# Kernel optimization log

Measured on AMD Instinct MI355X. Metric: run time of the kernel, lower is better.

The kernel has to match this reference:

```python
import jax, jax.numpy as jnp
import numpy as np

N_NODES = 50000
N_EDGES = 800000
D = 64
LN_EPS = 1e-5


def setup_inputs() -> dict:
    key = jax.random.key(0)
    k1, k2, k3 = jax.random.split(key, 3)
    x = jax.random.normal(k1, (N_NODES, D), dtype=jnp.float32)
    edge_index = jax.random.randint(k2, (2, N_EDGES), 0, N_NODES, dtype=jnp.int64)
    # GCNConv linear weight (no bias in lin; conv bias separate), kaiming-ish scale
    W = jax.random.normal(k3, (D, D), dtype=jnp.float32) / np.sqrt(D)
    b = jnp.zeros((D,), dtype=jnp.float32)
    # LayerNorm affine params
    gamma = jnp.ones((D,), dtype=jnp.float32)
    beta = jnp.zeros((D,), dtype=jnp.float32)
    return {"x": x, "edge_index": edge_index, "W": W, "b": b, "gamma": gamma, "beta": beta}


def reference(x, edge_index, W, b, gamma, beta):
    n = x.shape[0]
    # --- GCNConv (normalize=True, improved=False, add_self_loops=True) ---
    loops = jnp.arange(n, dtype=edge_index.dtype)
    src = jnp.concatenate([edge_index[0], loops])  # message sources j
    dst = jnp.concatenate([edge_index[1], loops])  # message targets i
    ew = jnp.ones(src.shape[0], dtype=x.dtype)
    deg = jax.ops.segment_sum(ew, dst, num_segments=n)          # in-degree incl. self-loop
    dinv = jnp.where(deg > 0, jax.lax.rsqrt(jnp.where(deg > 0, deg, 1.0)), 0.0)
    norm = dinv[src] * dinv[dst]                                 # [E+N]
    xw = x @ W                                                   # [N, D]
    z = jax.ops.segment_sum(norm[:, None] * xw[src], dst, num_segments=n) + b
    # --- identity skip connection ---
    h = x + z
    # --- norm_act_drop: LayerNorm + ReLU (dropout_prob=0) ---
    mu = jnp.mean(h, axis=-1, keepdims=True)
    var = jnp.mean((h - mu) ** 2, axis=-1, keepdims=True)
    hn = (h - mu) * jax.lax.rsqrt(var + LN_EPS)
    return jax.nn.relu(hn * gamma + beta)
```

## Files before the change

### kernel.cpp

```cpp
#include <hip/hip_runtime.h>
#include <hip/hip_fp16.h>

#define N_NODES 50000
#define N_EDGES 800000
#define D 64
#define LN_EPS 1e-5f
#define CAP 48
#define SENT 50000
#define PREP_NB ((N_EDGES / 4 + 255) / 256)
#define GEMM_NB ((N_NODES + 63) / 64)
#define CNT_PAD 50048
#define XS_ROWS 50008
#define NCHK 98
#define CHSZ 8192
#define HALF 25000
#define SC_EB 782

typedef unsigned short u16;
typedef unsigned int u32;


__global__ __launch_bounds__(256) void prep_gemm_k(const int* __restrict__ src,
                                                   const int* __restrict__ dst,
                                                   u32* __restrict__ pe,
                                                   const float* __restrict__ x,
                                                   const float* __restrict__ W,
                                                   __half* __restrict__ xs) {
    __shared__ float xlds[D * D];
    int bid = blockIdx.x;
    int tid = threadIdx.x;
    if (bid < PREP_NB) {
        int gid = bid * 256 + tid;
        if (gid < N_EDGES / 4) {
            int4 s = ((const int4*)src)[gid];
            int4 d = ((const int4*)dst)[gid];
            uint4 p;
            p.x = (u32)(u16)d.x | ((u32)(u16)s.x << 16);
            p.y = (u32)(u16)d.y | ((u32)(u16)s.y << 16);
            p.z = (u32)(u16)d.z | ((u32)(u16)s.z << 16);
            p.w = (u32)(u16)d.w | ((u32)(u16)s.w << 16);
            ((uint4*)pe)[gid] = p;
        }
    } else {
        int row0 = (bid - PREP_NB) * 64;
        const float4* xg = (const float4*)(x + (size_t)row0 * D);
        float4* xl4 = (float4*)xlds;
        for (int i = tid; i < D * D / 4; i += 256) {
            int grow = row0 + (i >> 4);
            xl4[i] = (grow < N_NODES) ? xg[i] : make_float4(0.f, 0.f, 0.f, 0.f);
        }
        int lane = tid & 63;
        float wcol[D];
#pragma unroll
        for (int k = 0; k < D; ++k) wcol[k] = W[k * D + lane];
        __syncthreads();
        int wv = tid >> 6;
        for (int rr = 0; rr < 16; ++rr) {
            int r = wv * 16 + rr;
            int grow = row0 + r;
            if (grow >= N_NODES + 1) break;
            const float4* xr = (const float4*)(xlds + r * D);
            float acc = 0.f;
#pragma unroll
            for (int k4 = 0; k4 < 16; ++k4) {
                float4 xv = xr[k4];
                acc += xv.x * wcol[k4 * 4 + 0];
                acc += xv.y * wcol[k4 * 4 + 1];
                acc += xv.z * wcol[k4 * 4 + 2];
                acc += xv.w * wcol[k4 * 4 + 3];
            }
            xs[(size_t)grow * D + lane] = __float2half(acc);
        }
    }
}

__global__ __launch_bounds__(256) void hist_k(const u32* __restrict__ pe,
                                              u16* __restrict__ lpos,
                                              u16* __restrict__ H) {
    __shared__ u32 lh[HALF / 2];
    int c = blockIdx.x >> 1;
    int r = blockIdx.x & 1;
    int rlo = r * HALF;
    for (int w = threadIdx.x; w < HALF / 2; w += 256) lh[w] = 0;
    __syncthreads();
    int cbase = c * CHSZ;
    u32* H32 = (u32*)H;
#pragma unroll 4
    for (int i = 0; i < CHSZ / 256; ++i) {
        int e = cbase + threadIdx.x + i * 256;
        if (e < N_EDGES) {
            u32 p = pe[e];
            int t = (int)(p & 0xffffu);
            unsigned tr = (unsigned)(t - rlo);
            if (tr < HALF) {
                u32 addend = (tr & 1) ? 0x10000u : 1u;
                u32 old = atomicAdd(&lh[tr >> 1], addend);
                u32 lp = (tr & 1) ? (old >> 16) : (old & 0xffffu);
                lpos[e] = (u16)lp;
            }
        }
    }
    __syncthreads();
    for (int w = threadIdx.x; w < HALF / 2; w += 256)
        H32[(size_t)c * (HALF) + r * (HALF / 2) + w] = lh[w];
}

__global__ __launch_bounds__(256) void pref_k(u16* __restrict__ H,
                                              int* __restrict__ cnt) {
    __shared__ u32 ph[NCHK * 128];
    int n0 = blockIdx.x * 256;
    int wbase = n0 >> 1;
    u32* H32 = (u32*)H;
    for (int idx = threadIdx.x; idx < NCHK * 128; idx += 256) {
        int c = idx >> 7, w = idx & 127;
        int gw = wbase + w;
        ph[idx] = (gw < HALF) ? H32[(size_t)c * HALF + gw] : 0;
    }
    __syncthreads();
    u16* ph16 = (u16*)ph;
    u32 run = 0;
    for (int c = 0; c < NCHK; ++c) {
        int off = c * 256 + threadIdx.x;
        u32 v = ph16[off];
        ph16[off] = (u16)run;
        run += v;
    }
    int n = n0 + threadIdx.x;
    if (n < N_NODES) cnt[n] = (int)run;
    __syncthreads();
    for (int idx = threadIdx.x; idx < NCHK * 128; idx += 256) {
        int c = idx >> 7, w = idx & 127;
        int gw = wbase + w;
        if (gw < HALF) H32[(size_t)c * HALF + gw] = ph[idx];
    }
}

__global__ __launch_bounds__(256) void scatter_scale_k(const u32* __restrict__ pe,
                                                       const u16* __restrict__ lpos,
                                                       const u16* __restrict__ H,
                                                       const int* __restrict__ cnt,
                                                       u16* __restrict__ ssrc,
                                                       __half* __restrict__ xs) {
    int bid = blockIdx.x;
    if (bid < SC_EB) {
        int e4 = bid * 1024 + threadIdx.x * 4;
        if (e4 >= N_EDGES) return;
        uint4 p = ((const uint4*)pe)[e4 >> 2];
        ushort4 lp = ((const ushort4*)lpos)[e4 >> 2];
        int c = e4 >> 13;
        const u16* st = H + (size_t)c * 50000;
        u32 pp[4] = {p.x, p.y, p.z, p.w};
        u16 ll[4] = {lp.x, lp.y, lp.z, lp.w};
#pragma unroll
        for (int k = 0; k < 4; ++k) {
            int t = (int)(pp[k] & 0xffffu);
            int pos = (int)st[t] + (int)ll[k];
            if (pos < CAP) ssrc[(size_t)t * CAP + pos] = (u16)(pp[k] >> 16);
        }
    } else {
        int gid = (bid - SC_EB) * 256 + threadIdx.x;
        if (gid >= N_NODES * 8) return;
        int row = gid >> 3;
        float di = rsqrtf((float)cnt[row] + 1.0f);
        float4 raw = ((const float4*)xs)[gid];
        __half2* hp = (__half2*)&raw;
#pragma unroll
        for (int i = 0; i < 4; ++i) {
            float2 f = __half22float2(hp[i]);
            hp[i] = __floats2half2_rn(di * f.x, di * f.y);
        }
        ((float4*)xs)[gid] = raw;
    }
}

__global__ __launch_bounds__(256) void agg_ln_k(
        const float* __restrict__ x, const __half* __restrict__ xs,
        const int* __restrict__ cnt, const u16* __restrict__ ssrc,
        const float* __restrict__ b, const float* __restrict__ gamma,
        const float* __restrict__ beta, float* __restrict__ out) {
    int row = blockIdx.x * 4 + (threadIdx.x >> 6);
    if (row >= N_NODES) return;
    int lane = threadIdx.x & 63;
    int sub = lane >> 3;
    int c8  = lane & 7;
    size_t base = (size_t)row * CAP;

    int dc = cnt[row];
    int s0 = ssrc[base + sub + 0];
    int s1 = ssrc[base + sub + 8];
    int s2 = ssrc[base + sub + 16];
    int s3 = ssrc[base + sub + 24];
    int s4 = ssrc[base + sub + 32];
    int s5 = ssrc[base + sub + 40];
    const float4* xp = (const float4*)(x + (size_t)row * D + c8 * 8);
    float4 x0 = xp[0], x1 = xp[1];
    float4 xsr = make_float4(0.f, 0.f, 0.f, 0.f);
    if (sub == 0) xsr = *(const float4*)(xs + (size_t)row * D + c8 * 8);

    int deg = dc < CAP ? dc : CAP;
    int ns = (deg + 7) >> 3;

    int v0 = (sub +  0 < deg) ? s0 : SENT;
    int v1 = (sub +  8 < deg) ? s1 : SENT;
    int v2 = (sub + 16 < deg) ? s2 : SENT;
    int v3 = (sub + 24 < deg) ? s3 : SENT;
    int v4 = (sub + 32 < deg) ? s4 : SENT;
    int v5 = (sub + 40 < deg) ? s5 : SENT;

    float4 r0 = make_float4(0.f,0.f,0.f,0.f), r1 = r0, r2 = r0,
           r3 = r0, r4 = r0, r5 = r0;
    if (0 < ns) r0 = *(const float4*)(xs + (size_t)v0 * D + c8 * 8);
    if (1 < ns) r1 = *(const float4*)(xs + (size_t)v1 * D + c8 * 8);
    if (2 < ns) r2 = *(const float4*)(xs + (size_t)v2 * D + c8 * 8);
    if (3 < ns) r3 = *(const float4*)(xs + (size_t)v3 * D + c8 * 8);
    if (4 < ns) r4 = *(const float4*)(xs + (size_t)v4 * D + c8 * 8);
    if (5 < ns) r5 = *(const float4*)(xs + (size_t)v5 * D + c8 * 8);

    float di = rsqrtf((float)dc + 1.0f);

    float4 a0 = make_float4(0.f, 0.f, 0.f, 0.f);
    float4 a1 = make_float4(0.f, 0.f, 0.f, 0.f);
    {
        float4 rr[7] = {r0, r1, r2, r3, r4, r5, xsr};
#pragma unroll
        for (int k = 0; k < 7; ++k) {
            const __half2* hp = (const __half2*)&rr[k];
            float2 p0 = __half22float2(hp[0]), p1 = __half22float2(hp[1]);
            float2 p2 = __half22float2(hp[2]), p3 = __half22float2(hp[3]);
            a0.x += p0.x; a0.y += p0.y; a0.z += p1.x; a0.w += p1.y;
            a1.x += p2.x; a1.y += p2.y; a1.z += p3.x; a1.w += p3.y;
        }
    }

#pragma unroll
    for (int o = 8; o < 64; o <<= 1) {
        a0.x += __shfl_xor(a0.x, o, 64); a0.y += __shfl_xor(a0.y, o, 64);
        a0.z += __shfl_xor(a0.z, o, 64); a0.w += __shfl_xor(a0.w, o, 64);
        a1.x += __shfl_xor(a1.x, o, 64); a1.y += __shfl_xor(a1.y, o, 64);
        a1.z += __shfl_xor(a1.z, o, 64); a1.w += __shfl_xor(a1.w, o, 64);
    }

    const float4* bp = (const float4*)(b + c8 * 8);
    float4 b0 = bp[0], b1 = bp[1];

    float h[8];
    h[0] = x0.x + di * a0.x + b0.x;
    h[1] = x0.y + di * a0.y + b0.y;
    h[2] = x0.z + di * a0.z + b0.z;
    h[3] = x0.w + di * a0.w + b0.w;
    h[4] = x1.x + di * a1.x + b1.x;
    h[5] = x1.y + di * a1.y + b1.y;
    h[6] = x1.z + di * a1.z + b1.z;
    h[7] = x1.w + di * a1.w + b1.w;

    float s_ = 0.f;
#pragma unroll
    for (int i = 0; i < 8; ++i) s_ += h[i];
#pragma unroll
    for (int o = 1; o < 64; o <<= 1) s_ += __shfl_xor(s_, o, 64);
    float mu = s_ * (1.0f / 512.0f);
    float v_ = 0.f;
    float dd[8];
#pragma unroll
    for (int i = 0; i < 8; ++i) { dd[i] = h[i] - mu; v_ += dd[i] * dd[i]; }
#pragma unroll
    for (int o = 1; o < 64; o <<= 1) v_ += __shfl_xor(v_, o, 64);
    float rstd = rsqrtf(v_ * (1.0f / 512.0f) + LN_EPS);

    if (sub == 0) {
        const float4* gp = (const float4*)(gamma + c8 * 8);
        const float4* ep = (const float4*)(beta + c8 * 8);
        float4 g0 = gp[0], g1 = gp[1];
        float4 e0 = ep[0], e1 = ep[1];
        float4 w0, w1;
        w0.x = fmaxf(dd[0] * rstd * g0.x + e0.x, 0.f);
        w0.y = fmaxf(dd[1] * rstd * g0.y + e0.y, 0.f);
        w0.z = fmaxf(dd[2] * rstd * g0.z + e0.z, 0.f);
        w0.w = fmaxf(dd[3] * rstd * g0.w + e0.w, 0.f);
        w1.x = fmaxf(dd[4] * rstd * g1.x + e1.x, 0.f);
        w1.y = fmaxf(dd[5] * rstd * g1.y + e1.y, 0.f);
        w1.z = fmaxf(dd[6] * rstd * g1.z + e1.z, 0.f);
        w1.w = fmaxf(dd[7] * rstd * g1.w + e1.w, 0.f);
        float4* op = (float4*)(out + (size_t)row * D + c8 * 8);
        op[0] = w0;
        op[1] = w1;
    }
}

extern "C" void kernel_launch(void* const* d_in, const int* in_sizes, int n_in,
                              void* d_out, int out_size, void* d_ws, size_t ws_size,
                              hipStream_t stream) {
    const float* x     = (const float*)d_in[0];
    const int*   ei    = (const int*)d_in[1];
    const float* W     = (const float*)d_in[2];
    const float* b     = (const float*)d_in[3];
    const float* gamma = (const float*)d_in[4];
    const float* beta  = (const float*)d_in[5];
    float* out = (float*)d_out;

    const int* src = ei;
    const int* dst = ei + N_EDGES;

    int*    cnt  = (int*)d_ws;
    __half* xs   = (__half*)(cnt + CNT_PAD);
    u32*    pe   = (u32*)(xs + (size_t)XS_ROWS * D);
    u16*    ssrc = (u16*)(pe + N_EDGES);
    u16*    H    = ssrc + (size_t)N_NODES * CAP;
    u16*    lpos = H + (size_t)NCHK * 50000;

    prep_gemm_k<<<PREP_NB + GEMM_NB, 256, 0, stream>>>(src, dst, pe, x, W, xs);
    hist_k<<<NCHK * 2, 256, 0, stream>>>(pe, lpos, H);
    pref_k<<<(N_NODES + 255) / 256, 256, 0, stream>>>(H, cnt);
    scatter_scale_k<<<SC_EB + (N_NODES * 8 + 255) / 256, 256, 0, stream>>>(
        pe, lpos, H, cnt, ssrc, xs);
    agg_ln_k<<<(N_NODES + 3) / 4, 256, 0, stream>>>(x, xs, cnt, ssrc, b, gamma, beta, out);
}
```

Baseline: 175.1 us.

## Repartition histogram into 8 node ranges by 64 chunks and simplify prefix scan

```diff
diff --git a/kernel.cpp b/kernel.cpp
--- a/kernel.cpp
+++ b/kernel.cpp
@@ -11,9 +11,10 @@
 #define GEMM_NB ((N_NODES + 63) / 64)
 #define CNT_PAD 50048
 #define XS_ROWS 50008
-#define NCHK 98
-#define CHSZ 8192
-#define HALF 25000
+#define NRG 8
+#define RSPAN2 6250
+#define NCH2 64
+#define CHSZ2 12500
 #define SC_EB 782
 
 typedef unsigned short u16;
@@ -77,61 +78,46 @@
 __global__ __launch_bounds__(256) void hist_k(const u32* __restrict__ pe,
                                               u16* __restrict__ lpos,
                                               u16* __restrict__ H) {
-    __shared__ u32 lh[HALF / 2];
-    int c = blockIdx.x >> 1;
-    int r = blockIdx.x & 1;
-    int rlo = r * HALF;
-    for (int w = threadIdx.x; w < HALF / 2; w += 256) lh[w] = 0;
+    __shared__ u32 lh[RSPAN2];
+    int r = blockIdx.x & (NRG - 1);
+    int c = blockIdx.x >> 3;
+    int lo = r * RSPAN2;
+    for (int w = threadIdx.x; w < RSPAN2; w += 256) lh[w] = 0;
     __syncthreads();
-    int cbase = c * CHSZ;
-    u32* H32 = (u32*)H;
-#pragma unroll 4
-    for (int i = 0; i < CHSZ / 256; ++i) {
-        int e = cbase + threadIdx.x + i * 256;
-        if (e < N_EDGES) {
+    int cbase = c * CHSZ2;
+    for (int i = 0; i < 49; ++i) {
+        int e = cbase + i * 256 + threadIdx.x;
+        if (e < cbase + CHSZ2) {
             u32 p = pe[e];
-            int t = (int)(p & 0xffffu);
-            unsigned tr = (unsigned)(t - rlo);
-            if (tr < HALF) {
-                u32 addend = (tr & 1) ? 0x10000u : 1u;
-                u32 old = atomicAdd(&lh[tr >> 1], addend);
-                u32 lp = (tr & 1) ? (old >> 16) : (old & 0xffffu);
-                lpos[e] = (u16)lp;
+            unsigned tr = (p & 0xffffu) - (unsigned)lo;
+            if (tr < RSPAN2) {
+                u32 old = atomicAdd(&lh[tr], 1u);
+                lpos[e] = (u16)old;
             }
         }
     }
     __syncthreads();
-    for (int w = threadIdx.x; w < HALF / 2; w += 256)
-        H32[(size_t)c * (HALF) + r * (HALF / 2) + w] = lh[w];
+    u32* H32 = (u32*)(H + (size_t)c * N_NODES + lo);
+    for (int w = threadIdx.x; w < RSPAN2 / 2; w += 256)
+        H32[w] = (lh[2 * w] & 0xffffu) | (lh[2 * w + 1] << 16);
 }
 
 __global__ __launch_bounds__(256) void pref_k(u16* __restrict__ H,
                                               int* __restrict__ cnt) {
-    __shared__ u32 ph[NCHK * 128];
-    int n0 = blockIdx.x * 256;
-    int wbase = n0 >> 1;
-    u32* H32 = (u32*)H;
-    for (int idx = threadIdx.x; idx < NCHK * 128; idx += 256) {
-        int c = idx >> 7, w = idx & 127;
-        int gw = wbase + w;
-        ph[idx] = (gw < HALF) ? H32[(size_t)c * HALF + gw] : 0;
-    }
-    __syncthreads();
-    u16* ph16 = (u16*)ph;
+    int n = blockIdx.x * 256 + threadIdx.x;
+    bool ok = (n < N_NODES);
+    u32 v[NCH2];
+#pragma unroll
+    for (int c = 0; c < NCH2; ++c)
+        v[c] = ok ? (u32)H[(size_t)c * N_NODES + n] : 0;
     u32 run = 0;
-    for (int c = 0; c < NCHK; ++c) {
-        int off = c * 256 + threadIdx.x;
-        u32 v = ph16[off];
-        ph16[off] = (u16)run;
-        run += v;
-    }
-    int n = n0 + threadIdx.x;
-    if (n < N_NODES) cnt[n] = (int)run;
-    __syncthreads();
-    for (int idx = threadIdx.x; idx < NCHK * 128; idx += 256) {
-        int c = idx >> 7, w = idx & 127;
-        int gw = wbase + w;
-        if (gw < HALF) H32[(size_t)c * HALF + gw] = ph[idx];
+#pragma unroll
+    for (int c = 0; c < NCH2; ++c) { u32 t = v[c]; v[c] = run; run += t; }
+    if (ok) {
+#pragma unroll
+        for (int c = 0; c < NCH2; ++c)
+            H[(size_t)c * N_NODES + n] = (u16)v[c];
+        cnt[n] = (int)run;
     }
 }
 
@@ -147,8 +133,8 @@
         if (e4 >= N_EDGES) return;
         uint4 p = ((const uint4*)pe)[e4 >> 2];
         ushort4 lp = ((const ushort4*)lpos)[e4 >> 2];
-        int c = e4 >> 13;
-        const u16* st = H + (size_t)c * 50000;
+        int c = e4 / CHSZ2;
+        const u16* st = H + (size_t)c * N_NODES;
         u32 pp[4] = {p.x, p.y, p.z, p.w};
         u16 ll[4] = {lp.x, lp.y, lp.z, lp.w};
 #pragma unroll
@@ -306,10 +292,10 @@
     u32*    pe   = (u32*)(xs + (size_t)XS_ROWS * D);
     u16*    ssrc = (u16*)(pe + N_EDGES);
     u16*    H    = ssrc + (size_t)N_NODES * CAP;
-    u16*    lpos = H + (size_t)NCHK * 50000;
+    u16*    lpos = H + (size_t)NCH2 * N_NODES;
 
     prep_gemm_k<<<PREP_NB + GEMM_NB, 256, 0, stream>>>(src, dst, pe, x, W, xs);
-    hist_k<<<NCHK * 2, 256, 0, stream>>>(pe, lpos, H);
+    hist_k<<<NRG * NCH2, 256, 0, stream>>>(pe, lpos, H);
     pref_k<<<(N_NODES + 255) / 256, 256, 0, stream>>>(H, cnt);
     scatter_scale_k<<<SC_EB + (N_NODES * 8 + 255) / 256, 256, 0, stream>>>(
         pe, lpos, H, cnt, ssrc, xs);
```

Result: faster. 164.8 us (-5.9%).
